# Kernel optimization log

Measured on AMD Instinct MI355X. Metric: run time of the kernel, lower is better.

The kernel has to match this reference:

```python
import jax, jax.numpy as jnp
import numpy as np

B, D = 16384, 512


def setup_inputs() -> dict:
    key = jax.random.key(0)
    ks = jax.random.split(key, 7)
    s1 = 1.0 / np.sqrt(D + 1)
    s2 = 1.0 / np.sqrt(2 * D + 1)
    return {
        "t": jax.random.uniform(ks[0], (1,), dtype=jnp.float32),
        "z": jax.random.normal(ks[1], (B, D), dtype=jnp.float32),
        "logp_z": jnp.zeros((B, 1), dtype=jnp.float32),
        "W1": jax.random.normal(ks[2], (2 * D, D + 1), dtype=jnp.float32) * s1,
        "b1": jax.random.normal(ks[3], (2 * D,), dtype=jnp.float32) * s1,
        "W2": jax.random.normal(ks[4], (D, 2 * D + 1), dtype=jnp.float32) * s2,
        "b2": jax.random.normal(ks[5], (D,), dtype=jnp.float32) * s2,
    }


def reference(t, z, logp_z, W1, b1, W2, b2):
    # CNF dynamics: dz/dt = fc2(concat(relu(fc1(concat(z, t))), t))
    batch = z.shape[0]
    tt = jnp.full((batch, 1), t[0], dtype=z.dtype)
    x = jnp.concatenate([z, tt], axis=1)            # [B, D+1]
    h_pre = x @ W1.T + b1                           # [B, 2D]
    h = jax.nn.relu(h_pre)
    x2 = jnp.concatenate([h, tt], axis=1)           # [B, 2D+1]
    dz_dt = x2 @ W2.T + b2                          # [B, D]

    # Exact Jacobian trace of linear-relu-linear block (closed form of the
    # per-dim autograd loop in trace_df_dz):
    #   tr J = sum_h relu'(h_pre[:,h]) * (sum_i W2[i,h] * W1[h,i])
    W2h = W2[:, : 2 * D]                            # drop time column, [D, 2D]
    W1z = W1[:, :D]                                 # drop time column, [2D, D]
    c = jnp.sum(W2h.T * W1z, axis=1)                # [2D]
    mask = (h_pre > 0).astype(z.dtype)              # relu'
    trace = mask @ c                                # [B]
    dlogp_z_dt = -trace[:, None]                    # [B, 1]
    return dz_dt, dlogp_z_dt
```

## Files before the change

kernel.cpp:

```cpp
#include <hip/hip_runtime.h>
#include <stdint.h>

#define B_   16384
#define D_   512
#define N1_  1024
#define K1_  512
#define N2_  512
#define K2_  1024

#define DELTA     4e-3f
#define LIST_CAP  (1u << 21)
#define LCAP      1024u

typedef _Float16 f16x8 __attribute__((ext_vector_type(8)));
typedef float    f32x4 __attribute__((ext_vector_type(4)));

__device__ __forceinline__ void gl_lds16(const void* g, void* l) {
  __builtin_amdgcn_global_load_lds(
      (const __attribute__((address_space(1))) uint32_t*)g,
      (__attribute__((address_space(3))) uint32_t*)l, 16, 0, 0);
}

__global__ __launch_bounds__(256) void prep_conv(const float* __restrict__ z,
                                                 const float* __restrict__ t,
                                                 const float* __restrict__ W1,
                                                 const float* __restrict__ b1,
                                                 const float* __restrict__ W2,
                                                 const float* __restrict__ b2,
                                                 _Float16* __restrict__ zh,
                                                 _Float16* __restrict__ w1h,
                                                 _Float16* __restrict__ w2h,
                                                 float* __restrict__ bias1,
                                                 float* __restrict__ bias2,
                                                 float* __restrict__ cvec,
                                                 float* __restrict__ dlogp,
                                                 uint32_t* __restrict__ counter) {
  int blk = blockIdx.x, tid = threadIdx.x;
  if (blk < 8192) {
    int i = blk * 256 + tid;
    if (blk < 64) dlogp[i] = 0.f;
    if (i == 16384) *counter = 0;
    float4 v = ((const float4*)z)[i];
    union { _Float16 h[4]; ushort4 u; } H;
    H.h[0] = (_Float16)(v.x * 16.f);
    H.h[1] = (_Float16)(v.y * 16.f);
    H.h[2] = (_Float16)(v.z * 16.f);
    H.h[3] = (_Float16)(v.w * 16.f);
    ((ushort4*)zh)[i] = H.u;
  } else if (blk < 8192 + 2048) {
    int idx = (blk - 8192) * 256 + tid;
    int j = idx >> 9, k = idx & 511;
    w1h[idx] = (_Float16)(W1[(size_t)j * 513 + k] * 64.f);
  } else if (blk < 8192 + 4096) {
    int idx = (blk - 8192 - 2048) * 256 + tid;
    int i = idx >> 10, j = idx & 1023;
    w2h[idx] = (_Float16)W2[(size_t)i * 1025 + j];
  } else if (blk < 8192 + 4100) {
    int j = (blk - 8192 - 4096) * 256 + tid;
    float t0 = t[0];
    bias1[j] = b1[j] + t0 * W1[(size_t)j * 513 + 512];
    if (j < 512) bias2[j] = b2[j] + t0 * W2[(size_t)j * 1025 + 1024];
  } else {
    int wave = tid >> 6, lane = tid & 63;
    int j = (blk - 8192 - 4100) * 4 + wave;
    float s = 0.f;
    #pragma unroll
    for (int kk = 0; kk < 8; ++kk) {
      int k = lane + kk * 64;
      s += W2[(size_t)k * 1025 + j] * W1[(size_t)j * 513 + k];
    }
    #pragma unroll
    for (int off = 32; off > 0; off >>= 1) s += __shfl_xor(s, off);
    if (lane == 0) cvec[j] = s;
  }
}


__global__ __launch_bounds__(256, 4)
void gemm1_kernel(const _Float16* __restrict__ zh, const _Float16* __restrict__ w1h,
                  const float* __restrict__ bias1, const float* __restrict__ cvec,
                  _Float16* __restrict__ hOut, float* __restrict__ dlogp,
                  uint32_t* __restrict__ list, uint32_t* __restrict__ counter) {
  __shared__ __align__(16) char smem[32768];
  __shared__ uint32_t llist[LCAP];
  __shared__ uint32_t lcnt, lbase;
  _Float16* Ah0  = (_Float16*)smem;
  _Float16* Ah1  = (_Float16*)(smem + 8192);
  _Float16* Bh0  = (_Float16*)(smem + 16384);
  _Float16* Bh1  = (_Float16*)(smem + 24576);
  _Float16* hbuf = (_Float16*)smem;

  const int tid = threadIdx.x;
  const int lane = tid & 63, wave = tid >> 6;
  const int wm = wave >> 1, wn = wave & 1;
  const int q = lane >> 4, m16 = lane & 15;
  const int bm = blockIdx.x & 127, bn = blockIdx.x >> 7;

  if (tid == 0) lcnt = 0;

  const int c0 = tid, c1 = 256 + tid;
  const int r0 = c0 >> 2, kc0 = (c0 & 3) << 3;
  const int r1 = c1 >> 2, kc1 = (c1 & 3) << 3;
  const _Float16* zh0 = zh + (size_t)(bm * 128 + r0) * K1_ + kc0;
  const _Float16* zh1 = zh + (size_t)(bm * 128 + r1) * K1_ + kc1;
  const _Float16* wh0 = w1h + (size_t)(bn * 128 + r0) * K1_ + kc0;
  const _Float16* wh1 = w1h + (size_t)(bn * 128 + r1) * K1_ + kc1;

  f32x4 acc[4][4] = {};

  for (int k0 = 0; k0 < K1_; k0 += 64) {
    gl_lds16(zh0 + k0,      &Ah0[c0 * 8]);
    gl_lds16(zh1 + k0,      &Ah0[c1 * 8]);
    gl_lds16(zh0 + k0 + 32, &Ah1[c0 * 8]);
    gl_lds16(zh1 + k0 + 32, &Ah1[c1 * 8]);
    gl_lds16(wh0 + k0,      &Bh0[c0 * 8]);
    gl_lds16(wh1 + k0,      &Bh0[c1 * 8]);
    gl_lds16(wh0 + k0 + 32, &Bh1[c0 * 8]);
    gl_lds16(wh1 + k0 + 32, &Bh1[c1 * 8]);
    __syncthreads();
    {
      f16x8 ah[4], bh[4];
      #pragma unroll
      for (int mt = 0; mt < 4; ++mt)
        ah[mt] = *(const f16x8*)&Ah0[(wm * 64 + mt * 16 + m16) * 32 + q * 8];
      #pragma unroll
      for (int nt = 0; nt < 4; ++nt)
        bh[nt] = *(const f16x8*)&Bh0[(wn * 64 + nt * 16 + m16) * 32 + q * 8];
      #pragma unroll
      for (int mt = 0; mt < 4; ++mt)
        #pragma unroll
        for (int nt = 0; nt < 4; ++nt)
          acc[mt][nt] = __builtin_amdgcn_mfma_f32_16x16x32_f16(ah[mt], bh[nt], acc[mt][nt], 0, 0, 0);
    }
    {
      f16x8 ah[4], bh[4];
      #pragma unroll
      for (int mt = 0; mt < 4; ++mt)
        ah[mt] = *(const f16x8*)&Ah1[(wm * 64 + mt * 16 + m16) * 32 + q * 8];
      #pragma unroll
      for (int nt = 0; nt < 4; ++nt)
        bh[nt] = *(const f16x8*)&Bh1[(wn * 64 + nt * 16 + m16) * 32 + q * 8];
      #pragma unroll
      for (int mt = 0; mt < 4; ++mt)
        #pragma unroll
        for (int nt = 0; nt < 4; ++nt)
          acc[mt][nt] = __builtin_amdgcn_mfma_f32_16x16x32_f16(ah[mt], bh[nt], acc[mt][nt], 0, 0, 0);
    }
    __syncthreads();
  }

  float tr[16];
  #pragma unroll
  for (int i = 0; i < 16; ++i) tr[i] = 0.f;
  #pragma unroll
  for (int nt = 0; nt < 4; ++nt) {
    int coll = wn * 64 + nt * 16 + m16;
    int col = bn * 128 + coll;
    float cj = cvec[col];
    float bj = bias1[col];
    #pragma unroll
    for (int mt = 0; mt < 4; ++mt) {
      int rowl = wm * 64 + mt * 16 + q * 4;
      #pragma unroll
      for (int r = 0; r < 4; ++r) {
        float hp = acc[mt][nt][r] * (1.f / 1024.f) + bj;
        float h = hp > 0.f ? hp : 0.f;
        hbuf[(rowl + r) * 128 + coll] = (_Float16)h;
        if (hp > 0.f) tr[mt * 4 + r] += cj;
        if (__builtin_fabsf(hp) < DELTA) {
          uint32_t i = atomicAdd(&lcnt, 1u);
          if (i < LCAP)
            llist[i] = ((uint32_t)(bm * 128 + rowl + r) << 10) | (uint32_t)col |
                       (hp > 0.f ? 0x80000000u : 0u);
        }
      }
    }
  }
  #pragma unroll
  for (int off = 1; off < 16; off <<= 1)
    #pragma unroll
    for (int i = 0; i < 16; ++i) tr[i] += __shfl_xor(tr[i], off);
  if (m16 == 0) {
    #pragma unroll
    for (int mt = 0; mt < 4; ++mt)
      #pragma unroll
      for (int r = 0; r < 4; ++r)
        atomicAdd(&dlogp[bm * 128 + wm * 64 + mt * 16 + q * 4 + r], -tr[mt * 4 + r]);
  }

  __syncthreads();
  #pragma unroll
  for (int it = 0; it < 8; ++it) {
    int idx = it * 256 + tid;
    int row = idx >> 4, cc = idx & 15;
    *(uint4*)&hOut[(size_t)(bm * 128 + row) * N1_ + bn * 128 + cc * 8] =
        *(const uint4*)&hbuf[row * 128 + cc * 8];
  }

  if (tid == 0) {
    uint32_t n = lcnt < LCAP ? lcnt : LCAP;
    lbase = atomicAdd(counter, n);
  }
  __syncthreads();
  uint32_t n = lcnt < LCAP ? lcnt : LCAP;
  uint32_t base = lbase;
  for (uint32_t i = tid; i < n; i += 256) {
    uint32_t gi = base + i;
    if (gi < LIST_CAP) list[gi] = llist[i];
  }
}


__global__ __launch_bounds__(256)
void fixup_kernel(const float* __restrict__ z, const float* __restrict__ W1,
                  const float* __restrict__ bias1, const float* __restrict__ cvec,
                  const uint32_t* __restrict__ list, const uint32_t* __restrict__ counter,
                  float* __restrict__ dlogp) {
  uint32_t cnt = *counter;
  if (cnt > LIST_CAP) cnt = LIST_CAP;
  const int wid = (blockIdx.x * 256 + threadIdx.x) >> 6;
  const int lane = threadIdx.x & 63;
  const int nw = gridDim.x * 4;
  for (uint32_t i = wid; i < cnt; i += nw) {
    uint32_t e = list[i];
    int row = (int)((e >> 10) & 16383u);
    int col = (int)(e & 1023u);
    int oldm = (int)(e >> 31);
    float s = 0.f;
    #pragma unroll
    for (int it = 0; it < 8; ++it) {
      int k = it * 64 + lane;
      s += z[(size_t)row * 512 + k] * W1[(size_t)col * 513 + k];
    }
    #pragma unroll
    for (int off = 32; off > 0; off >>= 1) s += __shfl_xor(s, off);
    if (lane == 0) {
      float hp = s + bias1[col];
      int newm = hp > 0.f ? 1 : 0;
      if (newm != oldm)
        atomicAdd(&dlogp[row], oldm ? cvec[col] : -cvec[col]);
    }
  }
}


__global__ __launch_bounds__(256, 4)
void gemm2_kernel(const _Float16* __restrict__ h, const _Float16* __restrict__ w2,
                  const float* __restrict__ bias2, float* __restrict__ out) {
  __shared__ __align__(16) char smem[34048];
  _Float16* As0 = (_Float16*)smem;
  _Float16* As1 = (_Float16*)(smem + 8192);
  _Float16* Bs0 = (_Float16*)(smem + 16384);
  _Float16* Bs1 = (_Float16*)(smem + 24576);
  float*    sbuf = (float*)smem;

  const int tid = threadIdx.x;
  const int lane = tid & 63, wave = tid >> 6;
  const int wm = wave >> 1, wn = wave & 1;
  const int q = lane >> 4, m16 = lane & 15;
  const int bm = blockIdx.x & 127, bn = blockIdx.x >> 7;

  const int c0 = tid, c1 = 256 + tid;
  const int r0 = c0 >> 2, kc0 = (c0 & 3) << 3;
  const int r1 = c1 >> 2, kc1 = (c1 & 3) << 3;
  const _Float16* hA0 = h + (size_t)(bm * 128 + r0) * K2_ + kc0;
  const _Float16* hA1 = h + (size_t)(bm * 128 + r1) * K2_ + kc1;
  const _Float16* wB0 = w2 + (size_t)(bn * 128 + r0) * K2_ + kc0;
  const _Float16* wB1 = w2 + (size_t)(bn * 128 + r1) * K2_ + kc1;

  f32x4 acc[4][4] = {};

  for (int k0 = 0; k0 < K2_; k0 += 64) {
    gl_lds16(hA0 + k0,      &As0[c0 * 8]);
    gl_lds16(hA1 + k0,      &As0[c1 * 8]);
    gl_lds16(hA0 + k0 + 32, &As1[c0 * 8]);
    gl_lds16(hA1 + k0 + 32, &As1[c1 * 8]);
    gl_lds16(wB0 + k0,      &Bs0[c0 * 8]);
    gl_lds16(wB1 + k0,      &Bs0[c1 * 8]);
    gl_lds16(wB0 + k0 + 32, &Bs1[c0 * 8]);
    gl_lds16(wB1 + k0 + 32, &Bs1[c1 * 8]);
    __syncthreads();
    {
      f16x8 af[4], bf[4];
      #pragma unroll
      for (int mt = 0; mt < 4; ++mt)
        af[mt] = *(const f16x8*)&As0[(wm * 64 + mt * 16 + m16) * 32 + q * 8];
      #pragma unroll
      for (int nt = 0; nt < 4; ++nt)
        bf[nt] = *(const f16x8*)&Bs0[(wn * 64 + nt * 16 + m16) * 32 + q * 8];
      #pragma unroll
      for (int mt = 0; mt < 4; ++mt)
        #pragma unroll
        for (int nt = 0; nt < 4; ++nt)
          acc[mt][nt] = __builtin_amdgcn_mfma_f32_16x16x32_f16(af[mt], bf[nt], acc[mt][nt], 0, 0, 0);
    }
    {
      f16x8 af[4], bf[4];
      #pragma unroll
      for (int mt = 0; mt < 4; ++mt)
        af[mt] = *(const f16x8*)&As1[(wm * 64 + mt * 16 + m16) * 32 + q * 8];
      #pragma unroll
      for (int nt = 0; nt < 4; ++nt)
        bf[nt] = *(const f16x8*)&Bs1[(wn * 64 + nt * 16 + m16) * 32 + q * 8];
      #pragma unroll
      for (int mt = 0; mt < 4; ++mt)
        #pragma unroll
        for (int nt = 0; nt < 4; ++nt)
          acc[mt][nt] = __builtin_amdgcn_mfma_f32_16x16x32_f16(af[mt], bf[nt], acc[mt][nt], 0, 0, 0);
    }
    __syncthreads();
  }

  #pragma unroll
  for (int half = 0; half < 2; ++half) {
    if (wm == half) {
      #pragma unroll
      for (int nt = 0; nt < 4; ++nt) {
        int coll = wn * 64 + nt * 16 + m16;
        float bj = bias2[bn * 128 + coll];
        #pragma unroll
        for (int mt = 0; mt < 4; ++mt) {
          int rowl = mt * 16 + q * 4;
          #pragma unroll
          for (int r = 0; r < 4; ++r)
            sbuf[(rowl + r) * 132 + coll] = acc[mt][nt][r] + bj;
        }
      }
    }
    __syncthreads();
    #pragma unroll
    for (int it = 0; it < 8; ++it) {
      int idx = it * 256 + tid;
      int row = idx >> 5, c4 = idx & 31;
      *(uint4*)&out[(size_t)(bm * 128 + half * 64 + row) * N2_ + bn * 128 + c4 * 4] =
          *(const uint4*)&sbuf[row * 132 + c4 * 4];
    }
    __syncthreads();
  }
}


extern "C" void kernel_launch(void* const* d_in, const int* in_sizes, int n_in,
                              void* d_out, int out_size, void* d_ws, size_t ws_size,
                              hipStream_t stream) {
  const float* t  = (const float*)d_in[0];
  const float* z  = (const float*)d_in[1];
  const float* W1 = (const float*)d_in[3];
  const float* b1 = (const float*)d_in[4];
  const float* W2 = (const float*)d_in[5];
  const float* b2 = (const float*)d_in[6];

  float* out   = (float*)d_out;
  float* dlogp = out + (size_t)B_ * D_;

  char* ws = (char*)d_ws;
  _Float16* zhp   = (_Float16*)ws; ws += (size_t)B_ * K1_ * 2;
  _Float16* w1h   = (_Float16*)ws; ws += (size_t)N1_ * K1_ * 2;
  _Float16* w2h   = (_Float16*)ws; ws += (size_t)N2_ * K2_ * 2;
  float*    bias1 = (float*)ws;    ws += 1024 * 4;
  float*    bias2 = (float*)ws;    ws += 512 * 4;
  float*    cvec  = (float*)ws;    ws += 1024 * 4;
  uint32_t* counter = (uint32_t*)ws; ws += 256;
  uint32_t* list  = (uint32_t*)ws; ws += (size_t)LIST_CAP * 4;
  _Float16* hWs   = (_Float16*)ws; ws += (size_t)B_ * N1_ * 2;

  prep_conv<<<8192 + 4100 + 256, 256, 0, stream>>>(z, t, W1, b1, W2, b2, zhp, w1h, w2h,
                                                   bias1, bias2, cvec, dlogp, counter);
  gemm1_kernel<<<1024, 256, 0, stream>>>(zhp, w1h, bias1, cvec, hWs, dlogp, list, counter);
  fixup_kernel<<<2048, 256, 0, stream>>>(z, W1, bias1, cvec, list, counter, dlogp);
  gemm2_kernel<<<512, 256, 0, stream>>>(hWs, w2h, bias2, out);
}
```

Measured before the change: 182.4 us.

## Fuse both GEMMs into one kernel keeping z and hidden activations in LDS

Replaces the separate z-conversion, GEMM1 and GEMM2 kernels with a single fused kernel. Each 512-thread block loads a 64-row z tile into swizzled LDS as fp16 and computes the hidden layer in two 512-column chunks. Each chunk goes through ReLU into LDS and is immediately consumed by GEMM2, so the fp16 z and hidden-activation round trips through global memory go away. Weights are streamed straight from global/L2 into registers with a one-step prefetch, and the trace is reduced in LDS, which drops the dlogp atomics. The cost is only 256 blocks, which may underfill the 256 CUs, plus repeated weight traffic per block.

```diff
diff --git a/kernel.cpp b/kernel.cpp
--- a/kernel.cpp
+++ b/kernel.cpp
@@ -10,59 +10,37 @@
 
 #define DELTA     4e-3f
 #define LIST_CAP  (1u << 21)
-#define LCAP      1024u
+#define LCAP      2048u
 
 typedef _Float16 f16x8 __attribute__((ext_vector_type(8)));
+typedef _Float16 f16x4 __attribute__((ext_vector_type(4)));
 typedef float    f32x4 __attribute__((ext_vector_type(4)));
 
-__device__ __forceinline__ void gl_lds16(const void* g, void* l) {
-  __builtin_amdgcn_global_load_lds(
-      (const __attribute__((address_space(1))) uint32_t*)g,
-      (__attribute__((address_space(3))) uint32_t*)l, 16, 0, 0);
-}
-
-__global__ __launch_bounds__(256) void prep_conv(const float* __restrict__ z,
-                                                 const float* __restrict__ t,
-                                                 const float* __restrict__ W1,
-                                                 const float* __restrict__ b1,
-                                                 const float* __restrict__ W2,
-                                                 const float* __restrict__ b2,
-                                                 _Float16* __restrict__ zh,
-                                                 _Float16* __restrict__ w1h,
-                                                 _Float16* __restrict__ w2h,
-                                                 float* __restrict__ bias1,
-                                                 float* __restrict__ bias2,
-                                                 float* __restrict__ cvec,
-                                                 float* __restrict__ dlogp,
-                                                 uint32_t* __restrict__ counter) {
+__global__ __launch_bounds__(256) void prep_w(
+    const float* __restrict__ t,
+    const float* __restrict__ W1, const float* __restrict__ b1,
+    const float* __restrict__ W2, const float* __restrict__ b2,
+    _Float16* __restrict__ w1h, _Float16* __restrict__ w2h,
+    float* __restrict__ bias1, float* __restrict__ bias2,
+    float* __restrict__ cvec, uint32_t* __restrict__ counter) {
   int blk = blockIdx.x, tid = threadIdx.x;
-  if (blk < 8192) {
-    int i = blk * 256 + tid;
-    if (blk < 64) dlogp[i] = 0.f;
-    if (i == 16384) *counter = 0;
-    float4 v = ((const float4*)z)[i];
-    union { _Float16 h[4]; ushort4 u; } H;
-    H.h[0] = (_Float16)(v.x * 16.f);
-    H.h[1] = (_Float16)(v.y * 16.f);
-    H.h[2] = (_Float16)(v.z * 16.f);
-    H.h[3] = (_Float16)(v.w * 16.f);
-    ((ushort4*)zh)[i] = H.u;
-  } else if (blk < 8192 + 2048) {
-    int idx = (blk - 8192) * 256 + tid;
+  if (blk < 2048) {
+    int idx = blk * 256 + tid;
     int j = idx >> 9, k = idx & 511;
     w1h[idx] = (_Float16)(W1[(size_t)j * 513 + k] * 64.f);
-  } else if (blk < 8192 + 4096) {
-    int idx = (blk - 8192 - 2048) * 256 + tid;
+  } else if (blk < 4096) {
+    int idx = (blk - 2048) * 256 + tid;
     int i = idx >> 10, j = idx & 1023;
     w2h[idx] = (_Float16)W2[(size_t)i * 1025 + j];
-  } else if (blk < 8192 + 4100) {
-    int j = (blk - 8192 - 4096) * 256 + tid;
+  } else if (blk < 4100) {
+    int j = (blk - 4096) * 256 + tid;
     float t0 = t[0];
     bias1[j] = b1[j] + t0 * W1[(size_t)j * 513 + 512];
     if (j < 512) bias2[j] = b2[j] + t0 * W2[(size_t)j * 1025 + 1024];
+    if (j == 0) *counter = 0;
   } else {
     int wave = tid >> 6, lane = tid & 63;
-    int j = (blk - 8192 - 4100) * 4 + wave;
+    int j = (blk - 4100) * 4 + wave;
     float s = 0.f;
     #pragma unroll
     for (int kk = 0; kk < 8; ++kk) {
@@ -76,125 +54,157 @@
 }
 
 
-__global__ __launch_bounds__(256, 4)
-void gemm1_kernel(const _Float16* __restrict__ zh, const _Float16* __restrict__ w1h,
-                  const float* __restrict__ bias1, const float* __restrict__ cvec,
-                  _Float16* __restrict__ hOut, float* __restrict__ dlogp,
-                  uint32_t* __restrict__ list, uint32_t* __restrict__ counter) {
-  __shared__ __align__(16) char smem[32768];
+__global__ __launch_bounds__(512, 2) void fused_kernel(
+    const float* __restrict__ z,
+    const _Float16* __restrict__ w1h, const _Float16* __restrict__ w2h,
+    const float* __restrict__ bias1, const float* __restrict__ bias2,
+    const float* __restrict__ cvec,
+    float* __restrict__ out, float* __restrict__ dlogp,
+    uint32_t* __restrict__ list, uint32_t* __restrict__ counter) {
+  __shared__ __align__(16) _Float16 Az[64 * 512];
+  __shared__ __align__(16) _Float16 Hb[64 * 512];
   __shared__ uint32_t llist[LCAP];
+  __shared__ float redbuf[8][64];
   __shared__ uint32_t lcnt, lbase;
-  _Float16* Ah0  = (_Float16*)smem;
-  _Float16* Ah1  = (_Float16*)(smem + 8192);
-  _Float16* Bh0  = (_Float16*)(smem + 16384);
-  _Float16* Bh1  = (_Float16*)(smem + 24576);
-  _Float16* hbuf = (_Float16*)smem;
-
-  const int tid = threadIdx.x;
-  const int lane = tid & 63, wave = tid >> 6;
-  const int wm = wave >> 1, wn = wave & 1;
-  const int q = lane >> 4, m16 = lane & 15;
-  const int bm = blockIdx.x & 127, bn = blockIdx.x >> 7;
+
+  const int tid  = threadIdx.x;
+  const int lane = tid & 63, w = tid >> 6;
+  const int q    = lane >> 4, m16 = lane & 15;
+  const int sw   = m16 & 7;
+  const int bm   = blockIdx.x;
 
   if (tid == 0) lcnt = 0;
 
-  const int c0 = tid, c1 = 256 + tid;
-  const int r0 = c0 >> 2, kc0 = (c0 & 3) << 3;
-  const int r1 = c1 >> 2, kc1 = (c1 & 3) << 3;
-  const _Float16* zh0 = zh + (size_t)(bm * 128 + r0) * K1_ + kc0;
-  const _Float16* zh1 = zh + (size_t)(bm * 128 + r1) * K1_ + kc1;
-  const _Float16* wh0 = w1h + (size_t)(bn * 128 + r0) * K1_ + kc0;
-  const _Float16* wh1 = w1h + (size_t)(bn * 128 + r1) * K1_ + kc1;
-
-  f32x4 acc[4][4] = {};
-
-  for (int k0 = 0; k0 < K1_; k0 += 64) {
-    gl_lds16(zh0 + k0,      &Ah0[c0 * 8]);
-    gl_lds16(zh1 + k0,      &Ah0[c1 * 8]);
-    gl_lds16(zh0 + k0 + 32, &Ah1[c0 * 8]);
-    gl_lds16(zh1 + k0 + 32, &Ah1[c1 * 8]);
-    gl_lds16(wh0 + k0,      &Bh0[c0 * 8]);
-    gl_lds16(wh1 + k0,      &Bh0[c1 * 8]);
-    gl_lds16(wh0 + k0 + 32, &Bh1[c0 * 8]);
-    gl_lds16(wh1 + k0 + 32, &Bh1[c1 * 8]);
+  {
+    const float* zp = z + (size_t)bm * 64 * 512;
+    #pragma unroll
+    for (int i = 0; i < 16; ++i) {
+      int slot = i * 512 + tid;
+      int row = slot >> 7, u8 = slot & 127;
+      f32x4 v = *(const f32x4*)(zp + (size_t)row * 512 + u8 * 4);
+      f16x4 hv;
+      #pragma unroll
+      for (int r = 0; r < 4; ++r) hv[r] = (_Float16)(v[r] * 16.f);
+      int gp = (u8 >> 1) ^ (row & 7);
+      *(f16x4*)((char*)Az + row * 1024 + gp * 16 + (u8 & 1) * 8) = hv;
+    }
+  }
+  __syncthreads();
+
+  float tr[4] = {0.f, 0.f, 0.f, 0.f};
+  f32x4 acc2[4][4] = {};
+  const char* azb = (const char*)Az + m16 * 1024;
+  const char* hbb = (const char*)Hb + m16 * 1024;
+  char*       hbw = (char*)Hb;
+
+  for (int ch = 0; ch < 2; ++ch) {
+    f32x4 acc1[4][4] = {};
+    const _Float16* w1base = w1h + (size_t)(ch * 512 + w * 64 + m16) * 512 + q * 8;
+    f16x8 wf[4];
+    #pragma unroll
+    for (int nt = 0; nt < 4; ++nt) wf[nt] = *(const f16x8*)(w1base + nt * 8192);
+    #pragma unroll
+    for (int ks = 0; ks < 16; ++ks) {
+      f16x8 cw[4], zf[4];
+      #pragma unroll
+      for (int nt = 0; nt < 4; ++nt) {
+        cw[nt] = wf[nt];
+        if (ks < 15) wf[nt] = *(const f16x8*)(w1base + nt * 8192 + (ks + 1) * 32);
+      }
+      #pragma unroll
+      for (int mt = 0; mt < 4; ++mt)
+        zf[mt] = *(const f16x8*)(azb + mt * 16384 + (((ks * 4 + q) ^ sw) << 4));
+      __builtin_amdgcn_s_setprio(1);
+      #pragma unroll
+      for (int nt = 0; nt < 4; ++nt)
+        #pragma unroll
+        for (int mt = 0; mt < 4; ++mt)
+          acc1[mt][nt] = __builtin_amdgcn_mfma_f32_16x16x32_f16(cw[nt], zf[mt], acc1[mt][nt], 0, 0, 0);
+      __builtin_amdgcn_s_setprio(0);
+    }
+
+    #pragma unroll
+    for (int nt = 0; nt < 4; ++nt) {
+      int colc = w * 64 + nt * 16 + q * 4;
+      f32x4 b4 = *(const f32x4*)(bias1 + ch * 512 + colc);
+      f32x4 c4 = *(const f32x4*)(cvec  + ch * 512 + colc);
+      #pragma unroll
+      for (int mt = 0; mt < 4; ++mt) {
+        int row = mt * 16 + m16;
+        f16x4 hv;
+        #pragma unroll
+        for (int r = 0; r < 4; ++r) {
+          float hp = acc1[mt][nt][r] * (1.f / 1024.f) + b4[r];
+          hv[r] = (_Float16)(hp > 0.f ? hp : 0.f);
+          if (hp > 0.f) tr[mt] += c4[r];
+          if (__builtin_fabsf(hp) < DELTA) {
+            uint32_t i = atomicAdd(&lcnt, 1u);
+            if (i < LCAP)
+              llist[i] = ((uint32_t)(bm * 64 + row) << 10) | (uint32_t)(ch * 512 + colc + r) |
+                         (hp > 0.f ? 0x80000000u : 0u);
+          }
+        }
+        int gp = ((colc >> 3) ^ (row & 7));
+        *(f16x4*)(hbw + row * 1024 + gp * 16 + (q & 1) * 8) = hv;
+      }
+    }
     __syncthreads();
+
     {
-      f16x8 ah[4], bh[4];
-      #pragma unroll
-      for (int mt = 0; mt < 4; ++mt)
-        ah[mt] = *(const f16x8*)&Ah0[(wm * 64 + mt * 16 + m16) * 32 + q * 8];
-      #pragma unroll
-      for (int nt = 0; nt < 4; ++nt)
-        bh[nt] = *(const f16x8*)&Bh0[(wn * 64 + nt * 16 + m16) * 32 + q * 8];
-      #pragma unroll
-      for (int mt = 0; mt < 4; ++mt)
+      const _Float16* w2base = w2h + (size_t)(w * 64 + m16) * 1024 + ch * 512 + q * 8;
+      f16x8 wf2[4];
+      #pragma unroll
+      for (int nt = 0; nt < 4; ++nt) wf2[nt] = *(const f16x8*)(w2base + nt * 16384);
+      #pragma unroll
+      for (int ks = 0; ks < 16; ++ks) {
+        f16x8 cw[4], hf[4];
+        #pragma unroll
+        for (int nt = 0; nt < 4; ++nt) {
+          cw[nt] = wf2[nt];
+          if (ks < 15) wf2[nt] = *(const f16x8*)(w2base + nt * 16384 + (ks + 1) * 32);
+        }
+        #pragma unroll
+        for (int mt = 0; mt < 4; ++mt)
+          hf[mt] = *(const f16x8*)(hbb + mt * 16384 + (((ks * 4 + q) ^ sw) << 4));
+        __builtin_amdgcn_s_setprio(1);
         #pragma unroll
         for (int nt = 0; nt < 4; ++nt)
-          acc[mt][nt] = __builtin_amdgcn_mfma_f32_16x16x32_f16(ah[mt], bh[nt], acc[mt][nt], 0, 0, 0);
-    }
-    {
-      f16x8 ah[4], bh[4];
-      #pragma unroll
-      for (int mt = 0; mt < 4; ++mt)
-        ah[mt] = *(const f16x8*)&Ah1[(wm * 64 + mt * 16 + m16) * 32 + q * 8];
-      #pragma unroll
-      for (int nt = 0; nt < 4; ++nt)
-        bh[nt] = *(const f16x8*)&Bh1[(wn * 64 + nt * 16 + m16) * 32 + q * 8];
-      #pragma unroll
-      for (int mt = 0; mt < 4; ++mt)
-        #pragma unroll
-        for (int nt = 0; nt < 4; ++nt)
-          acc[mt][nt] = __builtin_amdgcn_mfma_f32_16x16x32_f16(ah[mt], bh[nt], acc[mt][nt], 0, 0, 0);
+          #pragma unroll
+          for (int mt = 0; mt < 4; ++mt)
+            acc2[mt][nt] = __builtin_amdgcn_mfma_f32_16x16x32_f16(cw[nt], hf[mt], acc2[mt][nt], 0, 0, 0);
+        __builtin_amdgcn_s_setprio(0);
+      }
     }
     __syncthreads();
   }
 
-  float tr[16];
   #pragma unroll
-  for (int i = 0; i < 16; ++i) tr[i] = 0.f;
+  for (int mt = 0; mt < 4; ++mt) {
+    int row = bm * 64 + mt * 16 + m16;
+    #pragma unroll
+    for (int nt = 0; nt < 4; ++nt) {
+      int col = w * 64 + nt * 16 + q * 4;
+      f32x4 b2v = *(const f32x4*)(bias2 + col);
+      f32x4 v = acc2[mt][nt] + b2v;
+      *(f32x4*)(out + (size_t)row * 512 + col) = v;
+    }
+  }
+
   #pragma unroll
-  for (int nt = 0; nt < 4; ++nt) {
-    int coll = wn * 64 + nt * 16 + m16;
-    int col = bn * 128 + coll;
-    float cj = cvec[col];
-    float bj = bias1[col];
-    #pragma unroll
-    for (int mt = 0; mt < 4; ++mt) {
-      int rowl = wm * 64 + mt * 16 + q * 4;
-      #pragma unroll
-      for (int r = 0; r < 4; ++r) {
-        float hp = acc[mt][nt][r] * (1.f / 1024.f) + bj;
-        float h = hp > 0.f ? hp : 0.f;
-        hbuf[(rowl + r) * 128 + coll] = (_Float16)h;
-        if (hp > 0.f) tr[mt * 4 + r] += cj;
-        if (__builtin_fabsf(hp) < DELTA) {
-          uint32_t i = atomicAdd(&lcnt, 1u);
-          if (i < LCAP)
-            llist[i] = ((uint32_t)(bm * 128 + rowl + r) << 10) | (uint32_t)col |
-                       (hp > 0.f ? 0x80000000u : 0u);
-        }
-      }
-    }
-  }
-  #pragma unroll
-  for (int off = 1; off < 16; off <<= 1)
-    #pragma unroll
-    for (int i = 0; i < 16; ++i) tr[i] += __shfl_xor(tr[i], off);
-  if (m16 == 0) {
-    #pragma unroll
-    for (int mt = 0; mt < 4; ++mt)
-      #pragma unroll
-      for (int r = 0; r < 4; ++r)
-        atomicAdd(&dlogp[bm * 128 + wm * 64 + mt * 16 + q * 4 + r], -tr[mt * 4 + r]);
-  }
-
+  for (int mt = 0; mt < 4; ++mt) {
+    tr[mt] += __shfl_xor(tr[mt], 16);
+    tr[mt] += __shfl_xor(tr[mt], 32);
+  }
+  if (q == 0) {
+    #pragma unroll
+    for (int mt = 0; mt < 4; ++mt) redbuf[w][mt * 16 + m16] = tr[mt];
+  }
   __syncthreads();
-  #pragma unroll
-  for (int it = 0; it < 8; ++it) {
-    int idx = it * 256 + tid;
-    int row = idx >> 4, cc = idx & 15;
-    *(uint4*)&hOut[(size_t)(bm * 128 + row) * N1_ + bn * 128 + cc * 8] =
-        *(const uint4*)&hbuf[row * 128 + cc * 8];
+  if (tid < 64) {
+    float s = 0.f;
+    #pragma unroll
+    for (int ww = 0; ww < 8; ++ww) s += redbuf[ww][tid];
+    dlogp[bm * 64 + tid] = -s;
   }
 
   if (tid == 0) {
@@ -204,12 +214,11 @@
   __syncthreads();
   uint32_t n = lcnt < LCAP ? lcnt : LCAP;
   uint32_t base = lbase;
-  for (uint32_t i = tid; i < n; i += 256) {
+  for (uint32_t i = tid; i < n; i += 512) {
     uint32_t gi = base + i;
     if (gi < LIST_CAP) list[gi] = llist[i];
   }
 }
-
 
 __global__ __launch_bounds__(256)
 void fixup_kernel(const float* __restrict__ z, const float* __restrict__ W1,
@@ -243,103 +252,6 @@
   }
 }
 
-
-__global__ __launch_bounds__(256, 4)
-void gemm2_kernel(const _Float16* __restrict__ h, const _Float16* __restrict__ w2,
-                  const float* __restrict__ bias2, float* __restrict__ out) {
-  __shared__ __align__(16) char smem[34048];
-  _Float16* As0 = (_Float16*)smem;
-  _Float16* As1 = (_Float16*)(smem + 8192);
-  _Float16* Bs0 = (_Float16*)(smem + 16384);
-  _Float16* Bs1 = (_Float16*)(smem + 24576);
-  float*    sbuf = (float*)smem;
-
-  const int tid = threadIdx.x;
-  const int lane = tid & 63, wave = tid >> 6;
-  const int wm = wave >> 1, wn = wave & 1;
-  const int q = lane >> 4, m16 = lane & 15;
-  const int bm = blockIdx.x & 127, bn = blockIdx.x >> 7;
-
-  const int c0 = tid, c1 = 256 + tid;
-  const int r0 = c0 >> 2, kc0 = (c0 & 3) << 3;
-  const int r1 = c1 >> 2, kc1 = (c1 & 3) << 3;
-  const _Float16* hA0 = h + (size_t)(bm * 128 + r0) * K2_ + kc0;
-  const _Float16* hA1 = h + (size_t)(bm * 128 + r1) * K2_ + kc1;
-  const _Float16* wB0 = w2 + (size_t)(bn * 128 + r0) * K2_ + kc0;
-  const _Float16* wB1 = w2 + (size_t)(bn * 128 + r1) * K2_ + kc1;
-
-  f32x4 acc[4][4] = {};
-
-  for (int k0 = 0; k0 < K2_; k0 += 64) {
-    gl_lds16(hA0 + k0,      &As0[c0 * 8]);
-    gl_lds16(hA1 + k0,      &As0[c1 * 8]);
-    gl_lds16(hA0 + k0 + 32, &As1[c0 * 8]);
-    gl_lds16(hA1 + k0 + 32, &As1[c1 * 8]);
-    gl_lds16(wB0 + k0,      &Bs0[c0 * 8]);
-    gl_lds16(wB1 + k0,      &Bs0[c1 * 8]);
-    gl_lds16(wB0 + k0 + 32, &Bs1[c0 * 8]);
-    gl_lds16(wB1 + k0 + 32, &Bs1[c1 * 8]);
-    __syncthreads();
-    {
-      f16x8 af[4], bf[4];
-      #pragma unroll
-      for (int mt = 0; mt < 4; ++mt)
-        af[mt] = *(const f16x8*)&As0[(wm * 64 + mt * 16 + m16) * 32 + q * 8];
-      #pragma unroll
-      for (int nt = 0; nt < 4; ++nt)
-        bf[nt] = *(const f16x8*)&Bs0[(wn * 64 + nt * 16 + m16) * 32 + q * 8];
-      #pragma unroll
-      for (int mt = 0; mt < 4; ++mt)
-        #pragma unroll
-        for (int nt = 0; nt < 4; ++nt)
-          acc[mt][nt] = __builtin_amdgcn_mfma_f32_16x16x32_f16(af[mt], bf[nt], acc[mt][nt], 0, 0, 0);
-    }
-    {
-      f16x8 af[4], bf[4];
-      #pragma unroll
-      for (int mt = 0; mt < 4; ++mt)
-        af[mt] = *(const f16x8*)&As1[(wm * 64 + mt * 16 + m16) * 32 + q * 8];
-      #pragma unroll
-      for (int nt = 0; nt < 4; ++nt)
-        bf[nt] = *(const f16x8*)&Bs1[(wn * 64 + nt * 16 + m16) * 32 + q * 8];
-      #pragma unroll
-      for (int mt = 0; mt < 4; ++mt)
-        #pragma unroll
-        for (int nt = 0; nt < 4; ++nt)
-          acc[mt][nt] = __builtin_amdgcn_mfma_f32_16x16x32_f16(af[mt], bf[nt], acc[mt][nt], 0, 0, 0);
-    }
-    __syncthreads();
-  }
-
-  #pragma unroll
-  for (int half = 0; half < 2; ++half) {
-    if (wm == half) {
-      #pragma unroll
-      for (int nt = 0; nt < 4; ++nt) {
-        int coll = wn * 64 + nt * 16 + m16;
-        float bj = bias2[bn * 128 + coll];
-        #pragma unroll
-        for (int mt = 0; mt < 4; ++mt) {
-          int rowl = mt * 16 + q * 4;
-          #pragma unroll
-          for (int r = 0; r < 4; ++r)
-            sbuf[(rowl + r) * 132 + coll] = acc[mt][nt][r] + bj;
-        }
-      }
-    }
-    __syncthreads();
-    #pragma unroll
-    for (int it = 0; it < 8; ++it) {
-      int idx = it * 256 + tid;
-      int row = idx >> 5, c4 = idx & 31;
-      *(uint4*)&out[(size_t)(bm * 128 + half * 64 + row) * N2_ + bn * 128 + c4 * 4] =
-          *(const uint4*)&sbuf[row * 132 + c4 * 4];
-    }
-    __syncthreads();
-  }
-}
-
-
 extern "C" void kernel_launch(void* const* d_in, const int* in_sizes, int n_in,
                               void* d_out, int out_size, void* d_ws, size_t ws_size,
                               hipStream_t stream) {
@@ -354,7 +266,6 @@
   float* dlogp = out + (size_t)B_ * D_;
 
   char* ws = (char*)d_ws;
-  _Float16* zhp   = (_Float16*)ws; ws += (size_t)B_ * K1_ * 2;
   _Float16* w1h   = (_Float16*)ws; ws += (size_t)N1_ * K1_ * 2;
   _Float16* w2h   = (_Float16*)ws; ws += (size_t)N2_ * K2_ * 2;
   float*    bias1 = (float*)ws;    ws += 1024 * 4;
@@ -362,11 +273,8 @@
   float*    cvec  = (float*)ws;    ws += 1024 * 4;
   uint32_t* counter = (uint32_t*)ws; ws += 256;
   uint32_t* list  = (uint32_t*)ws; ws += (size_t)LIST_CAP * 4;
-  _Float16* hWs   = (_Float16*)ws; ws += (size_t)B_ * N1_ * 2;
-
-  prep_conv<<<8192 + 4100 + 256, 256, 0, stream>>>(z, t, W1, b1, W2, b2, zhp, w1h, w2h,
-                                                   bias1, bias2, cvec, dlogp, counter);
-  gemm1_kernel<<<1024, 256, 0, stream>>>(zhp, w1h, bias1, cvec, hWs, dlogp, list, counter);
+
+  prep_w<<<4356, 256, 0, stream>>>(t, W1, b1, W2, b2, w1h, w2h, bias1, bias2, cvec, counter);
+  fused_kernel<<<256, 512, 0, stream>>>(z, w1h, w2h, bias1, bias2, cvec, out, dlogp, list, counter);
   fixup_kernel<<<2048, 256, 0, stream>>>(z, W1, bias1, cvec, list, counter, dlogp);
-  gemm2_kernel<<<512, 256, 0, stream>>>(hWs, w2h, bias2, out);
-}
+}
```

Result: slower. 203.7 us (+11.6%).
